# Performance work log

Measured on AMD Instinct MI355X. Metric: run time of the kernel, lower is better.

The kernel has to match this reference:

```python
import jax, jax.numpy as jnp
import numpy as np

B, T, D, H = 2, 1024, 1024, 16
DH = D // H
_PAIRS = [(0, 1), (0, 2), (0, 3), (1, 2), (1, 3), (2, 3)]
_J6 = jnp.array([[0, 0, 0, 0, 0, 1],
                 [0, 0, 0, 0, -1, 0],
                 [0, 0, 0, 1, 0, 0],
                 [0, 0, 1, 0, 0, 0],
                 [0, -1, 0, 0, 0, 0],
                 [1, 0, 0, 0, 0, 0]], dtype=jnp.float32)


def exterior(p1, p2):
    # Plucker coordinates of the line through 4-vectors p1, p2, L2-normalized.
    parts = [p1[..., i] * p2[..., j] - p1[..., j] * p2[..., i] for i, j in _PAIRS]
    L = jnp.stack(parts, axis=-1)  # (..., 6)
    n = jnp.maximum(jnp.linalg.norm(L, axis=-1, keepdims=True), 1e-12)
    return L / n


def setup_inputs() -> dict:
    key = jax.random.key(0)
    ks = jax.random.split(key, 10)
    s = 0.02
    return {
        "x": jax.random.normal(ks[0], (B, T, D), jnp.float32),
        "Wqkv": jax.random.normal(ks[1], (3 * D, D), jnp.float32) * s,
        "bqkv": jnp.zeros((3 * D,), jnp.float32),
        "W1w": jax.random.normal(ks[2], (4 * H, D), jnp.float32) * s,
        "W2w": jax.random.normal(ks[3], (4 * H, D), jnp.float32) * s,
        "W1r": jax.random.normal(ks[4], (4 * H, D), jnp.float32) * s,
        "W2r": jax.random.normal(ks[5], (4 * H, D), jnp.float32) * s,
        "bias_scale": jnp.full((H,), 0.1, jnp.float32),
        "Wout": jax.random.normal(ks[6], (D, D), jnp.float32) * s,
        "bout": jnp.zeros((D,), jnp.float32),
    }


def reference(x, Wqkv, bqkv, W1w, W2w, W1r, W2r, bias_scale, Wout, bout):
    Bb, Tt, Dd = x.shape
    scale = DH ** (-0.5)
    qkv = (x @ Wqkv.T + bqkv).reshape(Bb, Tt, 3, H, DH)
    q = jnp.transpose(qkv[:, :, 0], (0, 2, 1, 3))  # (B,H,T,dh)
    k = jnp.transpose(qkv[:, :, 1], (0, 2, 1, 3))
    v = jnp.transpose(qkv[:, :, 2], (0, 2, 1, 3))
    std_logits = jnp.einsum('bhtd,bhsd->bhts', q, k) * scale

    x_prev = jnp.concatenate([jnp.zeros((Bb, 1, Dd), x.dtype), x[:, :-1]], axis=1)
    w1 = (x_prev @ W1w.T).reshape(Bb, Tt, H, 4)
    w2 = (x @ W2w.T).reshape(Bb, Tt, H, 4)
    write_lines = exterior(w1, w2)  # (B,T,H,6)
    r1 = (x @ W1r.T).reshape(Bb, Tt, H, 4)
    r2 = (x @ W2r.T).reshape(Bb, Tt, H, 4)
    read_lines = exterior(r1, r2)  # (B,T,H,6)

    Jw = jnp.einsum('bthi,ij->bhtj', write_lines, _J6)  # (B,H,T,6)
    rd = jnp.transpose(read_lines, (0, 2, 1, 3))        # (B,H,T,6)

    outer = Jw[..., :, None] * Jw[..., None, :]          # (B,H,T,6,6)
    M_causal = jnp.cumsum(outer, axis=2)                 # running Gram state
    rd_M = jnp.einsum('bhti,bhtij->bhtj', rd, M_causal)  # (B,H,T,6)
    bias_raw = jnp.einsum('bhti,bhsi->bhts', rd_M, Jw)   # (B,H,T,T)
    bias = jnp.abs(bias_raw) * bias_scale.reshape(1, H, 1, 1)

    logits = std_logits + bias
    mask = jnp.triu(jnp.ones((Tt, Tt), bool), 1)
    logits = jnp.where(mask, -jnp.inf, logits)
    attn = jax.nn.softmax(logits, axis=-1)
    out = jnp.einsum('bhts,bhsd->bthd', attn, v).reshape(Bb, Tt, Dd)
    return out @ Wout.T + bout
```

## Files before the change

### kernel.cpp

```cpp
#include <hip/hip_runtime.h>
#include <math.h>

#define B_ 2
#define T_ 1024
#define D_ 1024
#define H_ 16
#define NA_ 3328

typedef __attribute__((ext_vector_type(8))) short bf16x8;
typedef __attribute__((ext_vector_type(4))) float f32x4;

__device__ inline unsigned short f2bf(float x) {
  return (unsigned short)((__float_as_uint(x) + 0x8000u) >> 16);
}
__device__ inline unsigned bfpack(float lo, float hi) {
  unsigned a = __float_as_uint(hi) + 0x8000u;
  unsigned b = __float_as_uint(lo) + 0x8000u;
  return __builtin_amdgcn_perm(a, b, 0x07060302);
}
__device__ inline void hl_split(float x, unsigned short& h, unsigned short& l) {
  unsigned short hh = f2bf(x);
  float hf = __uint_as_float(((unsigned)hh) << 16);
  l = f2bf(x - hf);
  h = hh;
}

#define G_PRO()                                                                \
  const int tid = threadIdx.x;                                                 \
  const int w = tid >> 6, lane = tid & 63;                                     \
  const int lr = lane & 15, g = lane >> 4;                                     \
  const int wm = (w >> 1) * 64, wn = (w & 1) * 64;                             \
  const int row = tid >> 1, half = tid & 1;

#define G_LOADA(d, s) {                                                        \
  d[0] = *(const float4*)(Ap + (s) * 32);                                      \
  d[1] = *(const float4*)(Ap + (s) * 32 + 4);                                  \
  d[2] = *(const float4*)(Ap + (s) * 32 + 8);                                  \
  d[3] = *(const float4*)(Ap + (s) * 32 + 12); }
#define G_LOADB(d, s) {                                                        \
  d[0] = *(const float4*)(Bp + (s) * 32);                                      \
  d[1] = *(const float4*)(Bp + (s) * 32 + 4);                                  \
  d[2] = *(const float4*)(Bp + (s) * 32 + 8);                                  \
  d[3] = *(const float4*)(Bp + (s) * 32 + 12); }
#define G_STORE(bi, a, b) {                                                    \
  unsigned char* SA_ = Smem + (bi) * 8192;                                     \
  uint4 lo = make_uint4(bfpack(a[0].x, a[0].y), bfpack(a[0].z, a[0].w),        \
                        bfpack(a[1].x, a[1].y), bfpack(a[1].z, a[1].w));       \
  uint4 hi = make_uint4(bfpack(a[2].x, a[2].y), bfpack(a[2].z, a[2].w),        \
                        bfpack(a[3].x, a[3].y), bfpack(a[3].z, a[3].w));       \
  *(uint4*)(SA_ + (half * 2 + 0) * 2048 + row * 16) = lo;                      \
  *(uint4*)(SA_ + (half * 2 + 1) * 2048 + row * 16) = hi;                      \
  unsigned char* SB_ = Smem + 16384 + (bi) * 8192;                             \
  lo = make_uint4(bfpack(b[0].x, b[0].y), bfpack(b[0].z, b[0].w),              \
                  bfpack(b[1].x, b[1].y), bfpack(b[1].z, b[1].w));             \
  hi = make_uint4(bfpack(b[2].x, b[2].y), bfpack(b[2].z, b[2].w),              \
                  bfpack(b[3].x, b[3].y), bfpack(b[3].z, b[3].w));             \
  *(uint4*)(SB_ + (half * 2 + 0) * 2048 + row * 16) = lo;                      \
  *(uint4*)(SB_ + (half * 2 + 1) * 2048 + row * 16) = hi; }
#define G_COMPUTE(bi) {                                                        \
  const unsigned char* SA_ = Smem + (bi) * 8192;                               \
  const unsigned char* SB_ = Smem + 16384 + (bi) * 8192;                       \
  bf16x8 af[4], bfr[4];                                                        \
  _Pragma("unroll") for (int i = 0; i < 4; ++i)                                \
    af[i] = *(const bf16x8*)(SA_ + g * 2048 + (wm + i * 16 + lr) * 16);        \
  _Pragma("unroll") for (int j = 0; j < 4; ++j)                                \
    bfr[j] = *(const bf16x8*)(SB_ + g * 2048 + (wn + j * 16 + lr) * 16);       \
  _Pragma("unroll") for (int i = 0; i < 4; ++i)                                \
  _Pragma("unroll") for (int j = 0; j < 4; ++j)                                \
    acc[i][j] = __builtin_amdgcn_mfma_f32_16x16x32_bf16(af[i], bfr[j],         \
                                                        acc[i][j], 0, 0, 0); }
#define G_MAIN()                                                               \
  f32x4 acc[4][4];                                                             \
  const f32x4 zf = {0.f, 0.f, 0.f, 0.f};                                       \
  _Pragma("unroll") for (int i = 0; i < 4; ++i)                                \
  _Pragma("unroll") for (int j = 0; j < 4; ++j) acc[i][j] = zf;                \
  float4 a0[4], b0[4], a1[4], b1[4];                                           \
  G_LOADA(a0, 0); G_LOADB(b0, 0);                                              \
  G_STORE(0, a0, b0);                                                          \
  G_LOADA(a1, 1); G_LOADB(b1, 1);                                              \
  __syncthreads();                                                             \
  _Pragma("unroll 1") for (int s = 0; s < 32; s += 2) {                        \
    G_COMPUTE(0);                                                              \
    G_STORE(1, a1, b1);                                                        \
    if (s + 2 < 32) { G_LOADA(a0, s + 2); G_LOADB(b0, s + 2); }                \
    __syncthreads();                                                           \
    G_COMPUTE(1);                                                              \
    if (s + 2 < 32) G_STORE(0, a0, b0);                                        \
    if (s + 3 < 32) { G_LOADA(a1, s + 3); G_LOADB(b1, s + 3); }                \
    __syncthreads();                                                           \
  }

__global__ __launch_bounds__(256) void gemm_qkv(
    const float* __restrict__ A, const float* __restrict__ Wqkv,
    const float* __restrict__ bqkv,
    const float* __restrict__ W1w, const float* __restrict__ W2w,
    const float* __restrict__ W1r, const float* __restrict__ W2r,
    float* __restrict__ C)
{
  __shared__ __align__(16) unsigned char Smem[32768];
  const int m0 = blockIdx.y * 128, n0 = blockIdx.x * 128;
  G_PRO();
  const float* Ap = A + (size_t)(m0 + row) * 1024 + half * 16;
  const float* Bp;
  {
    const int cg = n0 + row;
    if (cg < 3072) Bp = Wqkv + (size_t)cg * 1024;
    else {
      const int r2 = cg - 3072;
      const float* Wm = (r2 < 64) ? W1w : (r2 < 128) ? W2w : (r2 < 192) ? W1r : W2r;
      Bp = Wm + (size_t)(r2 & 63) * 1024;
    }
    Bp += half * 16;
  }
  G_MAIN();
#pragma unroll
  for (int i = 0; i < 4; ++i) {
    const int rbase = m0 + wm + i * 16 + 4 * g;
#pragma unroll
    for (int j = 0; j < 4; ++j) {
      const int col = n0 + wn + j * 16 + lr;
      const float bb = (col < 3072) ? bqkv[col] : 0.f;
#pragma unroll
      for (int r = 0; r < 4; ++r)
        C[(size_t)(rbase + r) * NA_ + col] = acc[i][j][r] + bb;
    }
  }
}

__global__ __launch_bounds__(256) void gemm_out(
    const float* __restrict__ A, const float* __restrict__ Bm,
    const float* __restrict__ bias, float* __restrict__ C)
{
  __shared__ __align__(16) unsigned char Smem[32768];
  const int m0 = blockIdx.y * 128, n0 = blockIdx.x * 128;
  G_PRO();
  const float* Ap = A + (size_t)(m0 + row) * 1024 + half * 16;
  const float* Bp = Bm + (size_t)(n0 + row) * 1024 + half * 16;
  G_MAIN();
#pragma unroll
  for (int i = 0; i < 4; ++i) {
    const int rbase = m0 + wm + i * 16 + 4 * g;
#pragma unroll
    for (int j = 0; j < 4; ++j) {
      const int col = n0 + wn + j * 16 + lr;
      const float bb = bias[col];
#pragma unroll
      for (int r = 0; r < 4; ++r)
        C[(size_t)(rbase + r) * 1024 + col] = acc[i][j][r] + bb;
    }
  }
}

__global__ __launch_bounds__(256) void exterior_kernel(
    const float* __restrict__ qkvp,
    float* __restrict__ Jw, float* __restrict__ rd,
    unsigned* __restrict__ Jwpk)
{
  const int i = blockIdx.x * 256 + threadIdx.x;
  const int h = i & 15;
  const int t = (i >> 4) & 1023;
  const int b = i >> 14;
  const size_t rowt = ((size_t)(b * T_) + t) * NA_;

  float4 p1w = make_float4(0.f, 0.f, 0.f, 0.f);
  if (t > 0) p1w = *(const float4*)(qkvp + rowt - NA_ + 3072 + h * 4);
  const float4 p2w = *(const float4*)(qkvp + rowt + 3136 + h * 4);
  const float4 p1r = *(const float4*)(qkvp + rowt + 3200 + h * 4);
  const float4 p2r = *(const float4*)(qkvp + rowt + 3264 + h * 4);

  const size_t base = ((size_t)(b * H_ + h) * T_ + t) * 6;
  {
    const float L0 = p1w.x * p2w.y - p1w.y * p2w.x;
    const float L1 = p1w.x * p2w.z - p1w.z * p2w.x;
    const float L2 = p1w.x * p2w.w - p1w.w * p2w.x;
    const float L3 = p1w.y * p2w.z - p1w.z * p2w.y;
    const float L4 = p1w.y * p2w.w - p1w.w * p2w.y;
    const float L5 = p1w.z * p2w.w - p1w.w * p2w.z;
    const float n = sqrtf(L0 * L0 + L1 * L1 + L2 * L2 + L3 * L3 + L4 * L4 + L5 * L5);
    const float inv = 1.f / fmaxf(n, 1e-12f);
    float jv[6] = {L5 * inv, -L4 * inv, L3 * inv, L2 * inv, -L1 * inv, L0 * inv};
#pragma unroll
    for (int k = 0; k < 6; ++k) Jw[base + k] = jv[k];
    unsigned short JH[6], JL[6];
#pragma unroll
    for (int k = 0; k < 6; ++k) hl_split(jv[k], JH[k], JL[k]);
    unsigned* jp = Jwpk + (((size_t)(b * H_ + h) * T_ + t) << 4);
    unsigned h01 = JH[0] | ((unsigned)JH[1] << 16);
    unsigned h23 = JH[2] | ((unsigned)JH[3] << 16);
    unsigned h45 = JH[4] | ((unsigned)JH[5] << 16);
    jp[0] = h01; jp[1] = h23; jp[2] = h45;
    jp[3] = JL[0] | ((unsigned)JL[1] << 16);
    jp[4] = JL[2] | ((unsigned)JL[3] << 16);
    jp[5] = JL[4] | ((unsigned)JL[5] << 16);
    jp[6] = h01; jp[7] = h23; jp[8] = h45;
#pragma unroll
    for (int k = 9; k < 16; ++k) jp[k] = 0;
  }
  {
    const float L0 = p1r.x * p2r.y - p1r.y * p2r.x;
    const float L1 = p1r.x * p2r.z - p1r.z * p2r.x;
    const float L2 = p1r.x * p2r.w - p1r.w * p2r.x;
    const float L3 = p1r.y * p2r.z - p1r.z * p2r.y;
    const float L4 = p1r.y * p2r.w - p1r.w * p2r.y;
    const float L5 = p1r.z * p2r.w - p1r.w * p2r.z;
    const float n = sqrtf(L0 * L0 + L1 * L1 + L2 * L2 + L3 * L3 + L4 * L4 + L5 * L5);
    const float inv = 1.f / fmaxf(n, 1e-12f);
    rd[base + 0] = L0 * inv;
    rd[base + 1] = L1 * inv;
    rd[base + 2] = L2 * inv;
    rd[base + 3] = L3 * inv;
    rd[base + 4] = L4 * inv;
    rd[base + 5] = L5 * inv;
  }
}

__global__ __launch_bounds__(256) void scan_kernel(
    const float* __restrict__ Jw, const float* __restrict__ rd,
    unsigned* __restrict__ rdMpk)
{
  __shared__ float sc[256][40];
  const int tid = threadIdx.x;
  const int bh = blockIdx.x;
  const float* Jb = Jw + (size_t)bh * T_ * 6;
  const float* Rb = rd + (size_t)bh * T_ * 6;
  const int t0 = tid * 4;

  float L[36], M[36];
#pragma unroll
  for (int i = 0; i < 36; ++i) L[i] = 0.f;
  for (int tt = 0; tt < 4; ++tt) {
    float j6[6];
#pragma unroll
    for (int i = 0; i < 6; ++i) j6[i] = Jb[(size_t)(t0 + tt) * 6 + i];
#pragma unroll
    for (int a = 0; a < 6; ++a)
#pragma unroll
      for (int c = 0; c < 6; ++c)
        L[a * 6 + c] = fmaf(j6[a], j6[c], L[a * 6 + c]);
  }
#pragma unroll
  for (int i = 0; i < 36; ++i) M[i] = L[i];
#pragma unroll
  for (int k = 0; k < 9; ++k)
    *(float4*)&sc[tid][k * 4] = make_float4(M[k*4], M[k*4+1], M[k*4+2], M[k*4+3]);
  __syncthreads();

  for (int off = 1; off < 256; off <<= 1) {
    float4 tmp[9];
    const bool act = (tid >= off);
    if (act) {
#pragma unroll
      for (int k = 0; k < 9; ++k) tmp[k] = *(const float4*)&sc[tid - off][k * 4];
    }
    __syncthreads();
    if (act) {
#pragma unroll
      for (int k = 0; k < 9; ++k) {
        M[k*4]   += tmp[k].x; M[k*4+1] += tmp[k].y;
        M[k*4+2] += tmp[k].z; M[k*4+3] += tmp[k].w;
      }
#pragma unroll
      for (int k = 0; k < 9; ++k)
        *(float4*)&sc[tid][k * 4] = make_float4(M[k*4], M[k*4+1], M[k*4+2], M[k*4+3]);
    }
    __syncthreads();
  }

  float Mp[36];
#pragma unroll
  for (int i = 0; i < 36; ++i) Mp[i] = M[i] - L[i];

  for (int tt = 0; tt < 4; ++tt) {
    const int t = t0 + tt;
    float j6[6], r6[6];
#pragma unroll
    for (int i = 0; i < 6; ++i) { j6[i] = Jb[(size_t)t * 6 + i]; r6[i] = Rb[(size_t)t * 6 + i]; }
#pragma unroll
    for (int a = 0; a < 6; ++a)
#pragma unroll
      for (int c = 0; c < 6; ++c)
        Mp[a * 6 + c] = fmaf(j6[a], j6[c], Mp[a * 6 + c]);
    float s6[6];
#pragma unroll
    for (int jj = 0; jj < 6; ++jj) {
      float s = 0.f;
#pragma unroll
      for (int a = 0; a < 6; ++a) s = fmaf(r6[a], Mp[a * 6 + jj], s);
      s6[jj] = s;
    }
    unsigned short hh[6], ll[6];
#pragma unroll
    for (int i = 0; i < 6; ++i) hl_split(s6[i], hh[i], ll[i]);
    unsigned* ob = rdMpk + (((size_t)bh * T_ + t) << 4);
    unsigned h01 = hh[0] | ((unsigned)hh[1] << 16);
    unsigned h23 = hh[2] | ((unsigned)hh[3] << 16);
    unsigned h45 = hh[4] | ((unsigned)hh[5] << 16);
    ob[0] = h01; ob[1] = h23; ob[2] = h45;
    ob[3] = h01; ob[4] = h23; ob[5] = h45;
    ob[6] = ll[0] | ((unsigned)ll[1] << 16);
    ob[7] = ll[2] | ((unsigned)ll[3] << 16);
    ob[8] = ll[4] | ((unsigned)ll[5] << 16);
#pragma unroll
    for (int i = 9; i < 16; ++i) ob[i] = 0;
  }
}

__global__ __launch_bounds__(256) void attn_mfma(
    const float* __restrict__ qkvp,
    const unsigned* __restrict__ Jwpk,
    const unsigned* __restrict__ rdMpk,
    const float* __restrict__ bias_scale,
    float* __restrict__ attnout)
{
  __shared__ __align__(16) unsigned char smem[40960];
  unsigned char* KT = smem;
  unsigned char* VT = smem + 16384;
  unsigned char* PB = smem + 32768;

  const int gid = blockIdx.x;
  const int bh = gid & 31;
  const int c = (gid < 256) ? (15 - (gid >> 5)) : ((gid - 256) >> 5);
  const int b = bh >> 4, h = bh & 15;
  const int tid = threadIdx.x;
  const int w = tid >> 6;
  const int lane = tid & 63;
  const int lr = lane & 15;
  const int g = lane >> 4;
  const int t0 = c * 64;
  const int nT = c + 1;

  const float* Rows = qkvp + (size_t)b * T_ * NA_ + h * 64;
  const size_t jb = (size_t)(b * H_ + h) * T_;

  bf16x8 qa[2];
  {
    const float* qp = Rows + (size_t)(t0 + w * 16 + lr) * NA_;
#pragma unroll
    for (int kb = 0; kb < 2; ++kb) {
      const float4 f0 = *(const float4*)(qp + kb * 32 + g * 8);
      const float4 f1 = *(const float4*)(qp + kb * 32 + g * 8 + 4);
      union { uint4 u; bf16x8 v; } qq;
      qq.u = make_uint4(bfpack(f0.x, f0.y), bfpack(f0.z, f0.w),
                        bfpack(f1.x, f1.y), bfpack(f1.z, f1.w));
      qa[kb] = qq.v;
    }
  }
  bf16x8 ra = *(const bf16x8*)(rdMpk + ((jb + t0 + w * 16 + lr) << 4) + g * 4);
  const float bsc = bias_scale[h];

  float m[4], lsum[4];
  f32x4 O[4];
  const f32x4 zf = {0.f, 0.f, 0.f, 0.f};
#pragma unroll
  for (int r = 0; r < 4; ++r) { m[r] = -1e30f; lsum[r] = 0.f; }
#pragma unroll
  for (int d = 0; d < 4; ++d) O[d] = zf;

  const int kr = tid >> 2, kc = tid & 3;
  const int sp = tid & 31, d8 = tid >> 5;

  float4 kA[4], vA0, vA1, vA2, vA3, kN[4], vN0, vN1, vN2, vN3;
  {
    const float* kp = Rows + (size_t)kr * NA_ + 1024 + kc * 16;
#pragma unroll
    for (int i = 0; i < 4; ++i) kA[i] = *(const float4*)(kp + i * 4);
    const float* vr = Rows + (size_t)(2 * sp) * NA_ + 2048 + d8 * 8;
    vA0 = *(const float4*)vr;         vA1 = *(const float4*)(vr + 4);
    vA2 = *(const float4*)(vr + NA_); vA3 = *(const float4*)(vr + NA_ + 4);
  }

  for (int ti = 0; ti < nT; ++ti) {
    const int s0 = ti * 64;
    const int buf = ti & 1;
    {
      unsigned char* kt = KT + buf * 8192;
      const float e[16] = {kA[0].x, kA[0].y, kA[0].z, kA[0].w,
                           kA[1].x, kA[1].y, kA[1].z, kA[1].w,
                           kA[2].x, kA[2].y, kA[2].z, kA[2].w,
                           kA[3].x, kA[3].y, kA[3].z, kA[3].w};
      const int swz = (kr & 7) << 4;
      uint4 w0, w1;
      w0.x = bfpack(e[0], e[1]);  w0.y = bfpack(e[2], e[3]);
      w0.z = bfpack(e[4], e[5]);  w0.w = bfpack(e[6], e[7]);
      w1.x = bfpack(e[8], e[9]);  w1.y = bfpack(e[10], e[11]);
      w1.z = bfpack(e[12], e[13]); w1.w = bfpack(e[14], e[15]);
      *(uint4*)(kt + kr * 128 + ((kc * 32) ^ swz))      = w0;
      *(uint4*)(kt + kr * 128 + ((kc * 32 + 16) ^ swz)) = w1;
    }
    {
      unsigned* vt = (unsigned*)(VT + buf * 8192);
      const float r0[8] = {vA0.x, vA0.y, vA0.z, vA0.w, vA1.x, vA1.y, vA1.z, vA1.w};
      const float r1[8] = {vA2.x, vA2.y, vA2.z, vA2.w, vA3.x, vA3.y, vA3.z, vA3.w};
#pragma unroll
      for (int i = 0; i < 8; ++i) {
        const int d = d8 * 8 + i;
        vt[d * 32 + (sp ^ ((d & 7) << 2))] = bfpack(r0[i], r1[i]);
      }
    }
    if (ti + 1 < nT) {
      const float* kp = Rows + (size_t)(s0 + 64 + kr) * NA_ + 1024 + kc * 16;
#pragma unroll
      for (int i = 0; i < 4; ++i) kN[i] = *(const float4*)(kp + i * 4);
      const float* vr = Rows + (size_t)(s0 + 64 + 2 * sp) * NA_ + 2048 + d8 * 8;
      vN0 = *(const float4*)vr;         vN1 = *(const float4*)(vr + 4);
      vN2 = *(const float4*)(vr + NA_); vN3 = *(const float4*)(vr + NA_ + 4);
    }
    __syncthreads();

    f32x4 S[4], Sb[4];
    const unsigned char* kt = KT + buf * 8192;
    __builtin_amdgcn_s_setprio(1);
#pragma unroll
    for (int cb = 0; cb < 4; ++cb) {
      const int srw = cb * 16 + lr;
      f32x4 a = zf;
#pragma unroll
      for (int kb = 0; kb < 2; ++kb) {
        const bf16x8 kf = *(const bf16x8*)(kt + srw * 128 + (((kb * 64) + 16 * g) ^ ((srw & 7) << 4)));
        a = __builtin_amdgcn_mfma_f32_16x16x32_bf16(qa[kb], kf, a, 0, 0, 0);
      }
      S[cb] = a;
      const bf16x8 jw = *(const bf16x8*)(Jwpk + ((jb + s0 + cb * 16 + lr) << 4) + g * 4);
      Sb[cb] = __builtin_amdgcn_mfma_f32_16x16x32_bf16(ra, jw, zf, 0, 0, 0);
    }
    __builtin_amdgcn_s_setprio(0);

    const bool diag = (s0 == t0);
    float logit[4][4];
#pragma unroll
    for (int cb = 0; cb < 4; ++cb) {
#pragma unroll
      for (int r = 0; r < 4; ++r) {
        float lg = S[cb][r] * 0.125f + fabsf(Sb[cb][r]) * bsc;
        if (diag && (cb * 16 + lr > w * 16 + 4 * g + r)) lg = -1e30f;
        logit[cb][r] = lg;
      }
    }
#pragma unroll
    for (int r = 0; r < 4; ++r) {
      float mx = fmaxf(fmaxf(logit[0][r], logit[1][r]), fmaxf(logit[2][r], logit[3][r]));
      mx = fmaxf(mx, __shfl_xor(mx, 1));
      mx = fmaxf(mx, __shfl_xor(mx, 2));
      mx = fmaxf(mx, __shfl_xor(mx, 4));
      mx = fmaxf(mx, __shfl_xor(mx, 8));
      const float nm = fmaxf(m[r], mx);
      const float sc = __expf(m[r] - nm);
      m[r] = nm;
      lsum[r] *= sc;
#pragma unroll
      for (int d = 0; d < 4; ++d) O[d][r] *= sc;
    }
#pragma unroll
    for (int cb = 0; cb < 4; ++cb) {
#pragma unroll
      for (int r = 0; r < 4; ++r) {
        const float p = __expf(logit[cb][r] - m[r]);
        lsum[r] += p;
        const int q = 4 * g + r;
        const int s = cb * 16 + lr;
        const int byte = w * 2048 + q * 128 + ((2 * s) ^ ((q & 7) << 4));
        *(unsigned short*)(PB + byte) = f2bf(p);
      }
    }
    asm volatile("s_waitcnt lgkmcnt(0)" ::: "memory");
    __builtin_amdgcn_sched_barrier(0);

    bf16x8 pa[2];
#pragma unroll
    for (int kb = 0; kb < 2; ++kb) {
      const int byte = w * 2048 + lr * 128 + (((kb * 64) + 16 * g) ^ ((lr & 7) << 4));
      pa[kb] = *(const bf16x8*)(PB + byte);
    }
    const unsigned char* vtb = VT + buf * 8192;
    __builtin_amdgcn_s_setprio(1);
#pragma unroll
    for (int db = 0; db < 4; ++db) {
      const int d = db * 16 + lr;
#pragma unroll
      for (int kb = 0; kb < 2; ++kb) {
        const int byte = d * 128 + (((kb * 64) + 16 * g) ^ ((d & 7) << 4));
        const bf16x8 vf = *(const bf16x8*)(vtb + byte);
        O[db] = __builtin_amdgcn_mfma_f32_16x16x32_bf16(pa[kb], vf, O[db], 0, 0, 0);
      }
    }
    __builtin_amdgcn_s_setprio(0);
#pragma unroll
    for (int i = 0; i < 4; ++i) kA[i] = kN[i];
    vA0 = vN0; vA1 = vN1; vA2 = vN2; vA3 = vN3;
  }

#pragma unroll
  for (int r = 0; r < 4; ++r) {
    float l = lsum[r];
    l += __shfl_xor(l, 1);
    l += __shfl_xor(l, 2);
    l += __shfl_xor(l, 4);
    l += __shfl_xor(l, 8);
    lsum[r] = 1.f / l;
  }
  {
    const int qb = w * 16 + 4 * g;
#pragma unroll
    for (int db = 0; db < 4; ++db) {
#pragma unroll
      for (int r = 0; r < 4; ++r) {
        const int t = t0 + qb + r;
        attnout[(size_t)(b * T_ + t) * 1024 + h * 64 + db * 16 + lr] = O[db][r] * lsum[r];
      }
    }
  }
}

extern "C" void kernel_launch(void* const* d_in, const int* in_sizes, int n_in,
                              void* d_out, int out_size, void* d_ws, size_t ws_size,
                              hipStream_t stream)
{
  (void)in_sizes; (void)n_in; (void)out_size; (void)ws_size;
  const float* x    = (const float*)d_in[0];
  const float* Wqkv = (const float*)d_in[1];
  const float* bqkv = (const float*)d_in[2];
  const float* W1w  = (const float*)d_in[3];
  const float* W2w  = (const float*)d_in[4];
  const float* W1r  = (const float*)d_in[5];
  const float* W2r  = (const float*)d_in[6];
  const float* bsc  = (const float*)d_in[7];
  const float* Wout = (const float*)d_in[8];
  const float* bout = (const float*)d_in[9];
  float* out = (float*)d_out;

  float*    qkvp    = (float*)d_ws;
  float*    Jw      = qkvp + (size_t)2048 * NA_;
  float*    rd      = Jw + 196608;
  unsigned* Jwpk    = (unsigned*)(rd + 196608);
  unsigned* rdMpk   = Jwpk + 524288;
  float*    attnout = (float*)(rdMpk + 524288);

  gemm_qkv<<<dim3(26, 16), 256, 0, stream>>>(
      x, Wqkv, bqkv, W1w, W2w, W1r, W2r, qkvp);
  exterior_kernel<<<dim3(B_ * T_ * H_ / 256), 256, 0, stream>>>(
      qkvp, Jw, rd, Jwpk);
  scan_kernel<<<dim3(B_ * H_), 256, 0, stream>>>(Jw, rd, rdMpk);
  attn_mfma<<<dim3(B_ * H_ * (T_ / 64)), 256, 0, stream>>>(
      qkvp, Jwpk, rdMpk, bsc, attnout);
  gemm_out<<<dim3(8, 16), 256, 0, stream>>>(attnout, Wout, bout, out);
}
```

Measured before the change: 128.9 us.

## Shrink GEMM M-tile, fuse exterior into scan, add lazy softmax rescale

Both GEMMs switch from 128x128 to 64x128 tiles with a new smem layout, doubling the grid so more CUs are busy. The separate exterior kernel is folded into the scan kernel, which now computes the write and read lines directly from the qkv buffer; this removes one launch and the Jw/rd intermediate buffers, at the cost of recomputing Jw in the second pass. The attention softmax now skips rescaling the running max unless some row's max grows by more than 8, trading extra branching for fewer exp and multiply operations.

```diff
diff --git a/kernel.cpp b/kernel.cpp
--- a/kernel.cpp
+++ b/kernel.cpp
@@ -25,68 +25,64 @@
   h = hh;
 }
 
-#define G_PRO()                                                                \
+#define H_PRO()                                                                \
   const int tid = threadIdx.x;                                                 \
   const int w = tid >> 6, lane = tid & 63;                                     \
   const int lr = lane & 15, g = lane >> 4;                                     \
-  const int wm = (w >> 1) * 64, wn = (w & 1) * 64;                             \
-  const int row = tid >> 1, half = tid & 1;
-
-#define G_LOADA(d, s) {                                                        \
+  const int wm = (w >> 1) * 32, wn = (w & 1) * 64;                             \
+  const int arow = tid & 63, aslot = tid >> 6;                                 \
+  const int brow = tid & 127, bs2 = (tid >> 7) * 2;
+
+#define H_LOADA(d, s) {                                                        \
   d[0] = *(const float4*)(Ap + (s) * 32);                                      \
-  d[1] = *(const float4*)(Ap + (s) * 32 + 4);                                  \
-  d[2] = *(const float4*)(Ap + (s) * 32 + 8);                                  \
-  d[3] = *(const float4*)(Ap + (s) * 32 + 12); }
-#define G_LOADB(d, s) {                                                        \
+  d[1] = *(const float4*)(Ap + (s) * 32 + 4); }
+#define H_LOADB(d, s) {                                                        \
   d[0] = *(const float4*)(Bp + (s) * 32);                                      \
   d[1] = *(const float4*)(Bp + (s) * 32 + 4);                                  \
   d[2] = *(const float4*)(Bp + (s) * 32 + 8);                                  \
   d[3] = *(const float4*)(Bp + (s) * 32 + 12); }
-#define G_STORE(bi, a, b) {                                                    \
-  unsigned char* SA_ = Smem + (bi) * 8192;                                     \
-  uint4 lo = make_uint4(bfpack(a[0].x, a[0].y), bfpack(a[0].z, a[0].w),        \
-                        bfpack(a[1].x, a[1].y), bfpack(a[1].z, a[1].w));       \
-  uint4 hi = make_uint4(bfpack(a[2].x, a[2].y), bfpack(a[2].z, a[2].w),        \
-                        bfpack(a[3].x, a[3].y), bfpack(a[3].z, a[3].w));       \
-  *(uint4*)(SA_ + (half * 2 + 0) * 2048 + row * 16) = lo;                      \
-  *(uint4*)(SA_ + (half * 2 + 1) * 2048 + row * 16) = hi;                      \
-  unsigned char* SB_ = Smem + 16384 + (bi) * 8192;                             \
-  lo = make_uint4(bfpack(b[0].x, b[0].y), bfpack(b[0].z, b[0].w),              \
-                  bfpack(b[1].x, b[1].y), bfpack(b[1].z, b[1].w));             \
-  hi = make_uint4(bfpack(b[2].x, b[2].y), bfpack(b[2].z, b[2].w),              \
-                  bfpack(b[3].x, b[3].y), bfpack(b[3].z, b[3].w));             \
-  *(uint4*)(SB_ + (half * 2 + 0) * 2048 + row * 16) = lo;                      \
-  *(uint4*)(SB_ + (half * 2 + 1) * 2048 + row * 16) = hi; }
-#define G_COMPUTE(bi) {                                                        \
-  const unsigned char* SA_ = Smem + (bi) * 8192;                               \
-  const unsigned char* SB_ = Smem + 16384 + (bi) * 8192;                       \
-  bf16x8 af[4], bfr[4];                                                        \
-  _Pragma("unroll") for (int i = 0; i < 4; ++i)                                \
-    af[i] = *(const bf16x8*)(SA_ + g * 2048 + (wm + i * 16 + lr) * 16);        \
+#define H_STORE(bi, a, b) {                                                    \
+  unsigned char* SA_ = As + (bi) * 4096;                                       \
+  *(uint4*)(SA_ + aslot * 1024 + arow * 16) =                                  \
+      make_uint4(bfpack(a[0].x, a[0].y), bfpack(a[0].z, a[0].w),               \
+                 bfpack(a[1].x, a[1].y), bfpack(a[1].z, a[1].w));              \
+  unsigned char* SB_ = Bs + (bi) * 8192;                                       \
+  *(uint4*)(SB_ + bs2 * 2048 + brow * 16) =                                    \
+      make_uint4(bfpack(b[0].x, b[0].y), bfpack(b[0].z, b[0].w),               \
+                 bfpack(b[1].x, b[1].y), bfpack(b[1].z, b[1].w));              \
+  *(uint4*)(SB_ + (bs2 + 1) * 2048 + brow * 16) =                              \
+      make_uint4(bfpack(b[2].x, b[2].y), bfpack(b[2].z, b[2].w),               \
+                 bfpack(b[3].x, b[3].y), bfpack(b[3].z, b[3].w)); }
+#define H_COMPUTE(bi) {                                                        \
+  const unsigned char* SA_ = As + (bi) * 4096;                                 \
+  const unsigned char* SB_ = Bs + (bi) * 8192;                                 \
+  bf16x8 af[2], bfr[4];                                                        \
+  _Pragma("unroll") for (int i = 0; i < 2; ++i)                                \
+    af[i] = *(const bf16x8*)(SA_ + g * 1024 + (wm + i * 16 + lr) * 16);        \
   _Pragma("unroll") for (int j = 0; j < 4; ++j)                                \
     bfr[j] = *(const bf16x8*)(SB_ + g * 2048 + (wn + j * 16 + lr) * 16);       \
-  _Pragma("unroll") for (int i = 0; i < 4; ++i)                                \
+  _Pragma("unroll") for (int i = 0; i < 2; ++i)                                \
   _Pragma("unroll") for (int j = 0; j < 4; ++j)                                \
     acc[i][j] = __builtin_amdgcn_mfma_f32_16x16x32_bf16(af[i], bfr[j],         \
                                                         acc[i][j], 0, 0, 0); }
-#define G_MAIN()                                                               \
-  f32x4 acc[4][4];                                                             \
+#define H_MAIN()                                                               \
+  f32x4 acc[2][4];                                                             \
   const f32x4 zf = {0.f, 0.f, 0.f, 0.f};                                       \
-  _Pragma("unroll") for (int i = 0; i < 4; ++i)                                \
+  _Pragma("unroll") for (int i = 0; i < 2; ++i)                                \
   _Pragma("unroll") for (int j = 0; j < 4; ++j) acc[i][j] = zf;                \
-  float4 a0[4], b0[4], a1[4], b1[4];                                           \
-  G_LOADA(a0, 0); G_LOADB(b0, 0);                                              \
-  G_STORE(0, a0, b0);                                                          \
-  G_LOADA(a1, 1); G_LOADB(b1, 1);                                              \
+  float4 a0[2], b0[4], a1[2], b1[4];                                           \
+  H_LOADA(a0, 0); H_LOADB(b0, 0);                                              \
+  H_STORE(0, a0, b0);                                                          \
+  H_LOADA(a1, 1); H_LOADB(b1, 1);                                              \
   __syncthreads();                                                             \
   _Pragma("unroll 1") for (int s = 0; s < 32; s += 2) {                        \
-    G_COMPUTE(0);                                                              \
-    G_STORE(1, a1, b1);                                                        \
-    if (s + 2 < 32) { G_LOADA(a0, s + 2); G_LOADB(b0, s + 2); }                \
+    H_COMPUTE(0);                                                              \
+    H_STORE(1, a1, b1);                                                        \
+    if (s + 2 < 32) { H_LOADA(a0, s + 2); H_LOADB(b0, s + 2); }                \
     __syncthreads();                                                           \
-    G_COMPUTE(1);                                                              \
-    if (s + 2 < 32) G_STORE(0, a0, b0);                                        \
-    if (s + 3 < 32) { G_LOADA(a1, s + 3); G_LOADB(b1, s + 3); }                \
+    H_COMPUTE(1);                                                              \
+    if (s + 2 < 32) H_STORE(0, a0, b0);                                        \
+    if (s + 3 < 32) { H_LOADA(a1, s + 3); H_LOADB(b1, s + 3); }                \
     __syncthreads();                                                           \
   }
 
@@ -97,24 +93,25 @@
     const float* __restrict__ W1r, const float* __restrict__ W2r,
     float* __restrict__ C)
 {
-  __shared__ __align__(16) unsigned char Smem[32768];
-  const int m0 = blockIdx.y * 128, n0 = blockIdx.x * 128;
-  G_PRO();
-  const float* Ap = A + (size_t)(m0 + row) * 1024 + half * 16;
+  __shared__ __align__(16) unsigned char As[2 * 4096];
+  __shared__ __align__(16) unsigned char Bs[2 * 8192];
+  const int m0 = blockIdx.y * 64, n0 = blockIdx.x * 128;
+  H_PRO();
+  const float* Ap = A + (size_t)(m0 + arow) * 1024 + aslot * 8;
   const float* Bp;
   {
-    const int cg = n0 + row;
+    const int cg = n0 + brow;
     if (cg < 3072) Bp = Wqkv + (size_t)cg * 1024;
     else {
       const int r2 = cg - 3072;
       const float* Wm = (r2 < 64) ? W1w : (r2 < 128) ? W2w : (r2 < 192) ? W1r : W2r;
       Bp = Wm + (size_t)(r2 & 63) * 1024;
     }
-    Bp += half * 16;
-  }
-  G_MAIN();
-#pragma unroll
-  for (int i = 0; i < 4; ++i) {
+    Bp += bs2 * 8;
+  }
+  H_MAIN();
+#pragma unroll
+  for (int i = 0; i < 2; ++i) {
     const int rbase = m0 + wm + i * 16 + 4 * g;
 #pragma unroll
     for (int j = 0; j < 4; ++j) {
@@ -131,14 +128,15 @@
     const float* __restrict__ A, const float* __restrict__ Bm,
     const float* __restrict__ bias, float* __restrict__ C)
 {
-  __shared__ __align__(16) unsigned char Smem[32768];
-  const int m0 = blockIdx.y * 128, n0 = blockIdx.x * 128;
-  G_PRO();
-  const float* Ap = A + (size_t)(m0 + row) * 1024 + half * 16;
-  const float* Bp = Bm + (size_t)(n0 + row) * 1024 + half * 16;
-  G_MAIN();
-#pragma unroll
-  for (int i = 0; i < 4; ++i) {
+  __shared__ __align__(16) unsigned char As[2 * 4096];
+  __shared__ __align__(16) unsigned char Bs[2 * 8192];
+  const int m0 = blockIdx.y * 64, n0 = blockIdx.x * 128;
+  H_PRO();
+  const float* Ap = A + (size_t)(m0 + arow) * 1024 + aslot * 8;
+  const float* Bp = Bm + (size_t)(n0 + brow) * 1024 + bs2 * 8;
+  H_MAIN();
+#pragma unroll
+  for (int i = 0; i < 2; ++i) {
     const int rbase = m0 + wm + i * 16 + 4 * g;
 #pragma unroll
     for (int j = 0; j < 4; ++j) {
@@ -151,25 +149,26 @@
   }
 }
 
-__global__ __launch_bounds__(256) void exterior_kernel(
+__global__ __launch_bounds__(256) void scan_kernel(
     const float* __restrict__ qkvp,
-    float* __restrict__ Jw, float* __restrict__ rd,
-    unsigned* __restrict__ Jwpk)
+    unsigned* __restrict__ Jwpk, unsigned* __restrict__ rdMpk)
 {
-  const int i = blockIdx.x * 256 + threadIdx.x;
-  const int h = i & 15;
-  const int t = (i >> 4) & 1023;
-  const int b = i >> 14;
-  const size_t rowt = ((size_t)(b * T_) + t) * NA_;
-
-  float4 p1w = make_float4(0.f, 0.f, 0.f, 0.f);
-  if (t > 0) p1w = *(const float4*)(qkvp + rowt - NA_ + 3072 + h * 4);
-  const float4 p2w = *(const float4*)(qkvp + rowt + 3136 + h * 4);
-  const float4 p1r = *(const float4*)(qkvp + rowt + 3200 + h * 4);
-  const float4 p2r = *(const float4*)(qkvp + rowt + 3264 + h * 4);
-
-  const size_t base = ((size_t)(b * H_ + h) * T_ + t) * 6;
-  {
+  __shared__ float sc[256][41];
+  const int tid = threadIdx.x;
+  const int bh = blockIdx.x;
+  const int b = bh >> 4, h = bh & 15;
+  const int t0 = tid * 4;
+
+  float L[36];
+#pragma unroll
+  for (int i = 0; i < 36; ++i) L[i] = 0.f;
+
+  for (int tt = 0; tt < 4; ++tt) {
+    const int t = t0 + tt;
+    const size_t rowt = ((size_t)(b * T_) + t) * NA_;
+    float4 p1w = make_float4(0.f, 0.f, 0.f, 0.f);
+    if (t > 0) p1w = *(const float4*)(qkvp + rowt - NA_ + 3072 + h * 4);
+    const float4 p2w = *(const float4*)(qkvp + rowt + 3136 + h * 4);
     const float L0 = p1w.x * p2w.y - p1w.y * p2w.x;
     const float L1 = p1w.x * p2w.z - p1w.z * p2w.x;
     const float L2 = p1w.x * p2w.w - p1w.w * p2w.x;
@@ -178,16 +177,14 @@
     const float L5 = p1w.z * p2w.w - p1w.w * p2w.z;
     const float n = sqrtf(L0 * L0 + L1 * L1 + L2 * L2 + L3 * L3 + L4 * L4 + L5 * L5);
     const float inv = 1.f / fmaxf(n, 1e-12f);
-    float jv[6] = {L5 * inv, -L4 * inv, L3 * inv, L2 * inv, -L1 * inv, L0 * inv};
-#pragma unroll
-    for (int k = 0; k < 6; ++k) Jw[base + k] = jv[k];
+    const float jv[6] = {L5 * inv, -L4 * inv, L3 * inv, L2 * inv, -L1 * inv, L0 * inv};
     unsigned short JH[6], JL[6];
 #pragma unroll
     for (int k = 0; k < 6; ++k) hl_split(jv[k], JH[k], JL[k]);
-    unsigned* jp = Jwpk + (((size_t)(b * H_ + h) * T_ + t) << 4);
-    unsigned h01 = JH[0] | ((unsigned)JH[1] << 16);
-    unsigned h23 = JH[2] | ((unsigned)JH[3] << 16);
-    unsigned h45 = JH[4] | ((unsigned)JH[5] << 16);
+    unsigned* jp = Jwpk + (((size_t)bh * T_ + t) << 4);
+    const unsigned h01 = JH[0] | ((unsigned)JH[1] << 16);
+    const unsigned h23 = JH[2] | ((unsigned)JH[3] << 16);
+    const unsigned h45 = JH[4] | ((unsigned)JH[5] << 16);
     jp[0] = h01; jp[1] = h23; jp[2] = h45;
     jp[3] = JL[0] | ((unsigned)JL[1] << 16);
     jp[4] = JL[2] | ((unsigned)JL[3] << 16);
@@ -195,56 +192,20 @@
     jp[6] = h01; jp[7] = h23; jp[8] = h45;
 #pragma unroll
     for (int k = 9; k < 16; ++k) jp[k] = 0;
-  }
-  {
-    const float L0 = p1r.x * p2r.y - p1r.y * p2r.x;
-    const float L1 = p1r.x * p2r.z - p1r.z * p2r.x;
-    const float L2 = p1r.x * p2r.w - p1r.w * p2r.x;
-    const float L3 = p1r.y * p2r.z - p1r.z * p2r.y;
-    const float L4 = p1r.y * p2r.w - p1r.w * p2r.y;
-    const float L5 = p1r.z * p2r.w - p1r.w * p2r.z;
-    const float n = sqrtf(L0 * L0 + L1 * L1 + L2 * L2 + L3 * L3 + L4 * L4 + L5 * L5);
-    const float inv = 1.f / fmaxf(n, 1e-12f);
-    rd[base + 0] = L0 * inv;
-    rd[base + 1] = L1 * inv;
-    rd[base + 2] = L2 * inv;
-    rd[base + 3] = L3 * inv;
-    rd[base + 4] = L4 * inv;
-    rd[base + 5] = L5 * inv;
-  }
-}
-
-__global__ __launch_bounds__(256) void scan_kernel(
-    const float* __restrict__ Jw, const float* __restrict__ rd,
-    unsigned* __restrict__ rdMpk)
-{
-  __shared__ float sc[256][40];
-  const int tid = threadIdx.x;
-  const int bh = blockIdx.x;
-  const float* Jb = Jw + (size_t)bh * T_ * 6;
-  const float* Rb = rd + (size_t)bh * T_ * 6;
-  const int t0 = tid * 4;
-
-  float L[36], M[36];
-#pragma unroll
-  for (int i = 0; i < 36; ++i) L[i] = 0.f;
-  for (int tt = 0; tt < 4; ++tt) {
-    float j6[6];
-#pragma unroll
-    for (int i = 0; i < 6; ++i) j6[i] = Jb[(size_t)(t0 + tt) * 6 + i];
 #pragma unroll
     for (int a = 0; a < 6; ++a)
 #pragma unroll
-      for (int c = 0; c < 6; ++c)
-        L[a * 6 + c] = fmaf(j6[a], j6[c], L[a * 6 + c]);
-  }
+      for (int c2 = 0; c2 < 6; ++c2)
+        L[a * 6 + c2] = fmaf(jv[a], jv[c2], L[a * 6 + c2]);
+  }
+
+  float M[36];
 #pragma unroll
   for (int i = 0; i < 36; ++i) M[i] = L[i];
 #pragma unroll
   for (int k = 0; k < 9; ++k)
     *(float4*)&sc[tid][k * 4] = make_float4(M[k*4], M[k*4+1], M[k*4+2], M[k*4+3]);
   __syncthreads();
-
   for (int off = 1; off < 256; off <<= 1) {
     float4 tmp[9];
     const bool act = (tid >= off);
@@ -272,29 +233,57 @@
 
   for (int tt = 0; tt < 4; ++tt) {
     const int t = t0 + tt;
-    float j6[6], r6[6];
-#pragma unroll
-    for (int i = 0; i < 6; ++i) { j6[i] = Jb[(size_t)t * 6 + i]; r6[i] = Rb[(size_t)t * 6 + i]; }
+    const size_t rowt = ((size_t)(b * T_) + t) * NA_;
+    float4 p1w = make_float4(0.f, 0.f, 0.f, 0.f);
+    if (t > 0) p1w = *(const float4*)(qkvp + rowt - NA_ + 3072 + h * 4);
+    const float4 p2w = *(const float4*)(qkvp + rowt + 3136 + h * 4);
+    const float4 p1r = *(const float4*)(qkvp + rowt + 3200 + h * 4);
+    const float4 p2r = *(const float4*)(qkvp + rowt + 3264 + h * 4);
+    float jv[6], rv[6];
+    {
+      const float L0 = p1w.x * p2w.y - p1w.y * p2w.x;
+      const float L1 = p1w.x * p2w.z - p1w.z * p2w.x;
+      const float L2 = p1w.x * p2w.w - p1w.w * p2w.x;
+      const float L3 = p1w.y * p2w.z - p1w.z * p2w.y;
+      const float L4 = p1w.y * p2w.w - p1w.w * p2w.y;
+      const float L5 = p1w.z * p2w.w - p1w.w * p2w.z;
+      const float n = sqrtf(L0*L0 + L1*L1 + L2*L2 + L3*L3 + L4*L4 + L5*L5);
+      const float inv = 1.f / fmaxf(n, 1e-12f);
+      jv[0] = L5*inv; jv[1] = -L4*inv; jv[2] = L3*inv;
+      jv[3] = L2*inv; jv[4] = -L1*inv; jv[5] = L0*inv;
+    }
+    {
+      const float L0 = p1r.x * p2r.y - p1r.y * p2r.x;
+      const float L1 = p1r.x * p2r.z - p1r.z * p2r.x;
+      const float L2 = p1r.x * p2r.w - p1r.w * p2r.x;
+      const float L3 = p1r.y * p2r.z - p1r.z * p2r.y;
+      const float L4 = p1r.y * p2r.w - p1r.w * p2r.y;
+      const float L5 = p1r.z * p2r.w - p1r.w * p2r.z;
+      const float n = sqrtf(L0*L0 + L1*L1 + L2*L2 + L3*L3 + L4*L4 + L5*L5);
+      const float inv = 1.f / fmaxf(n, 1e-12f);
+      rv[0] = L0*inv; rv[1] = L1*inv; rv[2] = L2*inv;
+      rv[3] = L3*inv; rv[4] = L4*inv; rv[5] = L5*inv;
+    }
 #pragma unroll
     for (int a = 0; a < 6; ++a)
 #pragma unroll
-      for (int c = 0; c < 6; ++c)
-        Mp[a * 6 + c] = fmaf(j6[a], j6[c], Mp[a * 6 + c]);
+      for (int c2 = 0; c2 < 6; ++c2)
+        Mp[a * 6 + c2] = fmaf(jv[a], jv[c2], Mp[a * 6 + c2]);
     float s6[6];
 #pragma unroll
     for (int jj = 0; jj < 6; ++jj) {
       float s = 0.f;
 #pragma unroll
-      for (int a = 0; a < 6; ++a) s = fmaf(r6[a], Mp[a * 6 + jj], s);
+      for (int a = 0; a < 6; ++a) s = fmaf(rv[a], Mp[a * 6 + jj], s);
       s6[jj] = s;
     }
     unsigned short hh[6], ll[6];
 #pragma unroll
     for (int i = 0; i < 6; ++i) hl_split(s6[i], hh[i], ll[i]);
     unsigned* ob = rdMpk + (((size_t)bh * T_ + t) << 4);
-    unsigned h01 = hh[0] | ((unsigned)hh[1] << 16);
-    unsigned h23 = hh[2] | ((unsigned)hh[3] << 16);
-    unsigned h45 = hh[4] | ((unsigned)hh[5] << 16);
+    const unsigned h01 = hh[0] | ((unsigned)hh[1] << 16);
+    const unsigned h23 = hh[2] | ((unsigned)hh[3] << 16);
+    const unsigned h45 = hh[4] | ((unsigned)hh[5] << 16);
     ob[0] = h01; ob[1] = h23; ob[2] = h45;
     ob[3] = h01; ob[4] = h23; ob[5] = h45;
     ob[6] = ll[0] | ((unsigned)ll[1] << 16);
@@ -436,6 +425,7 @@
         logit[cb][r] = lg;
       }
     }
+    float mxr[4];
 #pragma unroll
     for (int r = 0; r < 4; ++r) {
       float mx = fmaxf(fmaxf(logit[0][r], logit[1][r]), fmaxf(logit[2][r], logit[3][r]));
@@ -443,12 +433,21 @@
       mx = fmaxf(mx, __shfl_xor(mx, 2));
       mx = fmaxf(mx, __shfl_xor(mx, 4));
       mx = fmaxf(mx, __shfl_xor(mx, 8));
-      const float nm = fmaxf(m[r], mx);
-      const float sc = __expf(m[r] - nm);
-      m[r] = nm;
-      lsum[r] *= sc;
-#pragma unroll
-      for (int d = 0; d < 4; ++d) O[d][r] *= sc;
+      mxr[r] = mx;
+    }
+    bool need = false;
+#pragma unroll
+    for (int r = 0; r < 4; ++r) need = need || (mxr[r] > m[r] + 8.f);
+    if (__any(need)) {
+#pragma unroll
+      for (int r = 0; r < 4; ++r) {
+        const float nm = fmaxf(m[r], mxr[r]);
+        const float sc = __expf(m[r] - nm);
+        m[r] = nm;
+        lsum[r] *= sc;
+#pragma unroll
+        for (int d = 0; d < 4; ++d) O[d][r] *= sc;
+      }
     }
 #pragma unroll
     for (int cb = 0; cb < 4; ++cb) {
@@ -529,18 +528,14 @@
   float* out = (float*)d_out;
 
   float*    qkvp    = (float*)d_ws;
-  float*    Jw      = qkvp + (size_t)2048 * NA_;
-  float*    rd      = Jw + 196608;
-  unsigned* Jwpk    = (unsigned*)(rd + 196608);
+  unsigned* Jwpk    = (unsigned*)(qkvp + (size_t)2048 * NA_);
   unsigned* rdMpk   = Jwpk + 524288;
   float*    attnout = (float*)(rdMpk + 524288);
 
-  gemm_qkv<<<dim3(26, 16), 256, 0, stream>>>(
+  gemm_qkv<<<dim3(26, 32), 256, 0, stream>>>(
       x, Wqkv, bqkv, W1w, W2w, W1r, W2r, qkvp);
-  exterior_kernel<<<dim3(B_ * T_ * H_ / 256), 256, 0, stream>>>(
-      qkvp, Jw, rd, Jwpk);
-  scan_kernel<<<dim3(B_ * H_), 256, 0, stream>>>(Jw, rd, rdMpk);
+  scan_kernel<<<dim3(B_ * H_), 256, 0, stream>>>(qkvp, Jwpk, rdMpk);
   attn_mfma<<<dim3(B_ * H_ * (T_ / 64)), 256, 0, stream>>>(
       qkvp, Jwpk, rdMpk, bsc, attnout);
-  gemm_out<<<dim3(8, 16), 256, 0, stream>>>(attnout, Wout, bout, out);
-}
+  gemm_out<<<dim3(8, 32), 256, 0, stream>>>(attnout, Wout, bout, out);
+}
```

New measurement: 194.9 us. 51.3% more time.
